# Performance work log

Hardware: AMD Instinct MI355X
Metric: run time of the kernel (lower is better)

## Reference

```python
import jax, jax.numpy as jnp
import numpy as np

B, T, F, U = 256, 512, 128, 1024  # batch, seq_len, feature dim, lstm units


def setup_inputs() -> dict:
    key = jax.random.key(0)
    ks = jax.random.split(key, 11)
    s = jnp.float32(0.05)  # small init so tanh/sigmoid stay in useful range
    f32 = jnp.float32
    return {
        "input_tensor": jax.random.normal(ks[0], (B, T, F), f32),
        # encoder LSTM weights (keras gate order i,f,c,o packed along last axis)
        "enc_Wx": jax.random.normal(ks[1], (F, 4 * U), f32) * s,
        "enc_Wh": jax.random.normal(ks[2], (U, 4 * U), f32) * s,
        "enc_b": jax.random.normal(ks[3], (4 * U,), f32) * s,
        # decoder LSTMCell weights (input dim = U, since it is fed its own output)
        "dec_Wx": jax.random.normal(ks[4], (U, 4 * U), f32) * s,
        "dec_Wh": jax.random.normal(ks[5], (U, 4 * U), f32) * s,
        "dec_b": jax.random.normal(ks[6], (4 * U,), f32) * s,
        # dense1: U -> U with relu; dense2: U -> F linear
        "d1_W": jax.random.normal(ks[7], (U, U), f32) * s,
        "d1_b": jax.random.normal(ks[8], (U,), f32) * s,
        "d2_W": jax.random.normal(ks[9], (U, F), f32) * s,
        "d2_b": jax.random.normal(ks[10], (F,), f32) * s,
    }


def _lstm_step(Wx, Wh, b):
    """Standard keras LSTM cell step. Gate packing order: i, f, g(cand), o."""
    def step(carry, x_t):
        h, c = carry
        z = x_t @ Wx + h @ Wh + b  # [B, 4U]
        i, f, g, o = jnp.split(z, 4, axis=-1)
        c = jax.nn.sigmoid(f) * c + jax.nn.sigmoid(i) * jnp.tanh(g)
        h = jax.nn.sigmoid(o) * jnp.tanh(c)
        return (h, c), h
    return step


def reference(input_tensor, enc_Wx, enc_Wh, enc_b, dec_Wx, dec_Wh, dec_b,
              d1_W, d1_b, d2_W, d2_b):
    x = input_tensor
    b_sz, t_len = x.shape[0], x.shape[1]
    u = enc_Wh.shape[0]
    h0 = jnp.zeros((b_sz, u), x.dtype)

    # Encoder: run LSTM over time, keep only final (h, c) (return_state=True).
    (h, c), _ = jax.lax.scan(_lstm_step(enc_Wx, enc_Wh, enc_b), (h0, h0),
                             jnp.swapaxes(x, 0, 1))  # xs: [T, B, F]

    # Decoder: feed previous output back as input, T steps.
    dec_step = _lstm_step(dec_Wx, dec_Wh, dec_b)
    def dec(carry, _):
        x_in, hh, cc = carry
        (hh, cc), _ = dec_step((hh, cc), x_in)
        return (hh, hh, cc), hh  # next input is the new hidden output

    _, hs = jax.lax.scan(dec, (h, h, c), None, length=t_len)  # hs: [T, B, U]

    # Per-step projections, fused over all timesteps (same math as in-loop dense).
    y = jnp.maximum(hs @ d1_W + d1_b, 0.0) @ d2_W + d2_b  # [T, B, F]
    return jnp.swapaxes(y, 0, 1)  # [B, T, F]
```

## Files before the change

### kernel.cpp

```cpp
#include <hip/hip_runtime.h>
#include <hip/hip_bf16.h>
#include <math.h>
#include <stdio.h>


typedef __attribute__((ext_vector_type(8))) short short8;
typedef __attribute__((ext_vector_type(4))) float f32x4;

#define MFMA(a, b, c) __builtin_amdgcn_mfma_f32_16x16x32_bf16(a, b, c, 0, 0, 0)

__device__ __forceinline__ short f2bf(float f) {
  union { __hip_bfloat16 h; short s; } u;
  u.h = __float2bfloat16(f);
  return u.s;
}
__device__ __forceinline__ void split3(float x, short& a, short& b, short& c) {
  union { __hip_bfloat16 h; short s; } u;
  u.h = __float2bfloat16(x); a = u.s;
  float r1 = x - __bfloat162float(u.h);
  u.h = __float2bfloat16(r1); b = u.s;
  float r2 = r1 - __bfloat162float(u.h);
  u.h = __float2bfloat16(r2); c = u.s;
}
__device__ __forceinline__ float sigm(float x) { return 1.0f / (1.0f + expf(-x)); }

__global__ void pack_w(const float* __restrict__ a, const float* __restrict__ b,
                       short8* __restrict__ dst, int KC, int mode, int ncols,
                       int limbs) {
  int gid = blockIdx.x * 256 + threadIdx.x;
  int lane = gid & 63;
  int kc = (gid >> 6) % KC;
  int nt = gid / (KC * 64);
  int u16 = lane & 15, kq = lane >> 4;
  int kbase = kc * 32 + kq * 8;
  int col;
  if (mode <= 1) { int g = nt & 3, ub = nt >> 2; col = g * 1024 + ub * 16 + u16; }
  else col = nt * 16 + u16;
  short8 v0, v1, v2;
#pragma unroll
  for (int j = 0; j < 8; ++j) {
    int k = kbase + j;
    float x;
    if (mode == 0)      x = a[(size_t)k * 4096 + col] + b[(size_t)k * 4096 + col];
    else if (mode == 1) x = (k < 1024) ? a[(size_t)k * 4096 + col]
                                       : b[(size_t)(k - 1024) * 4096 + col];
    else                x = a[(size_t)k * ncols + col];
    short sa, sb, sc; split3(x, sa, sb, sc);
    v0[j] = sa; v1[j] = sb; v2[j] = sc;
  }
  if (limbs == 3) {
    size_t base = (size_t)(nt * KC + kc) * 3 * 64 + lane;
    dst[base] = v0; dst[base + 64] = v1; dst[base + 128] = v2;
  } else {
    dst[(size_t)(nt * KC + kc) * 64 + lane] = v0;
  }
}

__global__ void pack_x32(const float* __restrict__ src, short8* __restrict__ dst,
                         int t0) {
  int gid = blockIdx.x * 256 + threadIdx.x;
  int lane = gid & 63;
  int kx = (gid >> 6) & 3;
  int mt = (gid >> 8) & 15;
  int tloc = gid >> 12;
  int bb = mt * 16 + (lane & 15);
  int fb = kx * 32 + (lane >> 4) * 8;
  const float* s = src + ((size_t)bb * 512 + (t0 + tloc)) * 128 + fb;
  short8 v0, v1, v2;
#pragma unroll
  for (int j = 0; j < 8; ++j) {
    short sa, sb, sc; split3(s[j], sa, sb, sc);
    v0[j] = sa; v1[j] = sb; v2[j] = sc;
  }
  size_t base = (size_t)((tloc * 16 + mt) * 4 + kx) * 3 * 64 + lane;
  dst[base] = v0; dst[base + 64] = v1; dst[base + 128] = v2;
}

__global__ void zero_f(float* p, int n) {
  int i = blockIdx.x * 256 + threadIdx.x;
  if (i < n) p[i] = 0.f;
}

__global__ __launch_bounds__(512) void lstm_step(
    const short8* __restrict__ Ah, const short8* __restrict__ Ax,
    const short8* __restrict__ W, const float* __restrict__ bias,
    float* __restrict__ cst, short8* __restrict__ Hnext,
    short8* __restrict__ Hring, int KC) {
  int tid = threadIdx.x;
  int lane = tid & 63, wv = tid >> 6;
  int wr = wv & 3, wc = wv >> 2;
  int xcd = blockIdx.x & 7, idx = blockIdx.x >> 3;
  int mb = idx & 3, ub = xcd * 8 + (idx >> 2);
  int mt = mb * 4 + wr;
  int nt0 = ub * 4 + wc * 2, nt1 = nt0 + 1;
  const f32x4 z4 = {0.f, 0.f, 0.f, 0.f};
  f32x4 acc0 = z4, acc1 = z4;
  for (int kc = 0; kc < KC; ++kc) {
    const short8* Ap = (kc < 32)
        ? (Ah + ((size_t)(mt * 32 + kc) * 3) * 64 + lane)
        : (Ax + ((size_t)(mt * 4 + (kc - 32)) * 3) * 64 + lane);
    short8 a0 = Ap[0], a1 = Ap[64], a2 = Ap[128];
    const short8* Bp = W + ((size_t)(nt0 * KC + kc) * 3) * 64 + lane;
    const short8* Bq = W + ((size_t)(nt1 * KC + kc) * 3) * 64 + lane;
    short8 b00 = Bp[0], b01 = Bp[64], b02 = Bp[128];
    short8 b10 = Bq[0], b11 = Bq[64], b12 = Bq[128];
    acc0 = MFMA(a0, b00, acc0);  acc1 = MFMA(a0, b10, acc1);
    acc0 = MFMA(a0, b01, acc0);  acc1 = MFMA(a0, b11, acc1);
    acc0 = MFMA(a1, b00, acc0);  acc1 = MFMA(a1, b10, acc1);
    acc0 = MFMA(a1, b01, acc0);  acc1 = MFMA(a1, b11, acc1);
    acc0 = MFMA(a0, b02, acc0);  acc1 = MFMA(a0, b12, acc1);
    acc0 = MFMA(a2, b00, acc0);  acc1 = MFMA(a2, b10, acc1);
  }

  __shared__ float zt[64][68];
  int u16 = lane & 15, quad = lane >> 4;
  float bv0 = bias[(wc * 2 + 0) * 1024 + ub * 16 + u16];
  float bv1 = bias[(wc * 2 + 1) * 1024 + ub * 16 + u16];
#pragma unroll
  for (int r = 0; r < 4; ++r) {
    zt[wr * 16 + quad * 4 + r][(wc * 2 + 0) * 16 + u16] = acc0[r] + bv0;
    zt[wr * 16 + quad * 4 + r][(wc * 2 + 1) * 16 + u16] = acc1[r] + bv1;
  }
  __syncthreads();

  if (tid < 128) {
    int r = tid >> 1, s = tid & 1;
    int m = mb * 64 + r;
    int ubase = ub * 16 + s * 8;
    float* cp = cst + (size_t)m * 1024 + ubase;
    short8 h0, h1, h2;
#pragma unroll
    for (int j = 0; j < 8; ++j) {
      int uu = s * 8 + j;
      float iv = zt[r][uu];
      float fv = zt[r][16 + uu];
      float gv = zt[r][32 + uu];
      float ov = zt[r][48 + uu];
      float cn = sigm(fv) * cp[j] + sigm(iv) * tanhf(gv);
      cp[j] = cn;
      float hval = sigm(ov) * tanhf(cn);
      short sa, sb, sc; split3(hval, sa, sb, sc);
      h0[j] = sa; h1[j] = sb; h2[j] = sc;
    }
    int mtw = m >> 4, r16 = m & 15;
    int kcw = ubase >> 5, ko = ubase & 31;
    int lane_t = r16 + 16 * (ko >> 3);
    size_t base = ((size_t)(mtw * 32 + kcw) * 3) * 64 + lane_t;
    Hnext[base] = h0; Hnext[base + 64] = h1; Hnext[base + 128] = h2;
    if (Hring)
      Hring[(size_t)(mtw * 32 + kcw) * 64 + lane_t] = h0;
  }
}

__global__ __launch_bounds__(256) void proj(
    const short8* __restrict__ HS, const short8* __restrict__ W1,
    const float* __restrict__ b1, const short8* __restrict__ W2,
    const float* __restrict__ b2, float* __restrict__ out, int t0) {
  int tid = threadIdx.x;
  int lane = tid & 63, wv = tid >> 6;
  int wr = wv & 1, wc = wv >> 1;
  int tloc = blockIdx.x >> 2, mb = blockIdx.x & 3;
  int t = t0 + tloc;
  const short8* A = HS + (size_t)tloc * 16 * 32 * 64;
  int u16 = lane & 15, quad = lane >> 4;
  int mt0 = mb * 4 + wr * 2;
  __shared__ short a1f[4][8][512];
  const f32x4 z4 = {0.f, 0.f, 0.f, 0.f};
  f32x4 acc2[2][4];
#pragma unroll
  for (int i = 0; i < 2; ++i)
#pragma unroll
    for (int jj = 0; jj < 4; ++jj) acc2[i][jj] = z4;

  for (int q = 0; q < 4; ++q) {
    f32x4 acc1[2][8];
#pragma unroll
    for (int i = 0; i < 2; ++i)
#pragma unroll
      for (int n = 0; n < 8; ++n) acc1[i][n] = z4;
    for (int kc = 0; kc < 32; ++kc) {
      short8 av0 = A[(size_t)(mt0 * 32 + kc) * 64 + lane];
      short8 av1 = A[(size_t)((mt0 + 1) * 32 + kc) * 64 + lane];
#pragma unroll
      for (int n = 0; n < 8; ++n) {
        int nt = q * 16 + wc * 8 + n;
        short8 bv = W1[(size_t)(nt * 32 + kc) * 64 + lane];
        acc1[0][n] = MFMA(av0, bv, acc1[0][n]);
        acc1[1][n] = MFMA(av1, bv, acc1[1][n]);
      }
    }
    __syncthreads();
#pragma unroll
    for (int i = 0; i < 2; ++i)
#pragma unroll
      for (int n = 0; n < 8; ++n)
#pragma unroll
        for (int r = 0; r < 4; ++r) {
          int rl = wr * 32 + i * 16 + quad * 4 + r;
          int nloc = wc * 128 + n * 16 + u16;
          float v = fmaxf(acc1[i][n][r] + b1[q * 256 + nloc], 0.f);
          int mtl = rl >> 4, r16 = rl & 15;
          int kcl = nloc >> 5, ko = nloc & 31;
          a1f[mtl][kcl][(r16 + 16 * (ko >> 3)) * 8 + (ko & 7)] = f2bf(v);
        }
    __syncthreads();
    for (int kcl = 0; kcl < 8; ++kcl) {
      short8 av0 = *(const short8*)&a1f[wr * 2 + 0][kcl][lane * 8];
      short8 av1 = *(const short8*)&a1f[wr * 2 + 1][kcl][lane * 8];
#pragma unroll
      for (int jj = 0; jj < 4; ++jj) {
        int nt2 = wc * 4 + jj;
        short8 bv = W2[(size_t)(nt2 * 32 + q * 8 + kcl) * 64 + lane];
        acc2[0][jj] = MFMA(av0, bv, acc2[0][jj]);
        acc2[1][jj] = MFMA(av1, bv, acc2[1][jj]);
      }
    }
  }
#pragma unroll
  for (int i = 0; i < 2; ++i)
#pragma unroll
    for (int jj = 0; jj < 4; ++jj)
#pragma unroll
      for (int r = 0; r < 4; ++r) {
        int rl = wr * 32 + i * 16 + quad * 4 + r;
        int f = wc * 64 + jj * 16 + u16;
        int bb = mb * 64 + rl;
        out[((size_t)bb * 512 + t) * 128 + f] = acc2[i][jj][r] + b2[f];
      }
}

extern "C" void kernel_launch(void* const* d_in, const int* in_sizes, int n_in,
                              void* d_out, int out_size, void* d_ws, size_t ws_size,
                              hipStream_t stream) {
  const float* x     = (const float*)d_in[0];
  const float* encWx = (const float*)d_in[1];
  const float* encWh = (const float*)d_in[2];
  const float* encb  = (const float*)d_in[3];
  const float* decWx = (const float*)d_in[4];
  const float* decWh = (const float*)d_in[5];
  const float* decb  = (const float*)d_in[6];
  const float* d1W   = (const float*)d_in[7];
  const float* d1b   = (const float*)d_in[8];
  const float* d2W   = (const float*)d_in[9];
  const float* d2b   = (const float*)d_in[10];

  char* ws = (char*)d_ws;
  size_t off = 0;
  short8* Wenc = (short8*)(ws + off); off += (size_t)256 * 36 * 3 * 64 * 16;
  short8* Wdec = (short8*)(ws + off); off += (size_t)256 * 32 * 3 * 64 * 16;
  short8* W1   = (short8*)(ws + off); off += (size_t)64 * 32 * 64 * 16;
  short8* W2   = (short8*)(ws + off); off += (size_t)8 * 32 * 64 * 16;
  short8* Xr   = (short8*)(ws + off); off += (size_t)32 * 16 * 4 * 3 * 64 * 16;
  short8* Hb   = (short8*)(ws + off); off += (size_t)2 * 16 * 32 * 3 * 64 * 16;
  short8* Hring= (short8*)(ws + off); off += (size_t)32 * 16 * 32 * 64 * 16;
  float*  cst  = (float*)(ws + off);  off += (size_t)256 * 1024 * 4;
  (void)in_sizes; (void)n_in; (void)out_size;
  if (ws_size < off) {
    fprintf(stderr, "kernel_launch: ws_size=%zu < needed=%zu -- aborting launch\n",
            ws_size, off);
    return;
  }

  pack_w<<<2304, 256, 0, stream>>>(encWh, encWx, Wenc, 36, 1, 4096, 3);
  pack_w<<<2048, 256, 0, stream>>>(decWx, decWh, Wdec, 32, 0, 4096, 3);
  pack_w<<<512, 256, 0, stream>>>(d1W, nullptr, W1, 32, 2, 1024, 1);
  pack_w<<<64, 256, 0, stream>>>(d2W, nullptr, W2, 32, 3, 128, 1);
  zero_f<<<1536, 256, 0, stream>>>((float*)Hb, 16 * 32 * 3 * 64 * 8);
  zero_f<<<1024, 256, 0, stream>>>(cst, 256 * 1024);

  const size_t H3 = (size_t)16 * 32 * 3 * 64;
  const size_t XT = (size_t)16 * 4 * 3 * 64;
  const size_t HR = (size_t)16 * 32 * 64;

  for (int c = 0; c < 16; ++c) {
    pack_x32<<<512, 256, 0, stream>>>(x, Xr, c * 32);
    for (int i = 0; i < 32; ++i) {
      int t = c * 32 + i;
      lstm_step<<<256, 512, 0, stream>>>(Hb + (size_t)(t & 1) * H3, Xr + (size_t)i * XT,
                                         Wenc, encb, cst,
                                         Hb + (size_t)((t + 1) & 1) * H3, nullptr, 36);
    }
  }
  for (int c = 0; c < 16; ++c) {
    for (int i = 0; i < 32; ++i) {
      int d = c * 32 + i;
      lstm_step<<<256, 512, 0, stream>>>(Hb + (size_t)(d & 1) * H3, nullptr,
                                         Wdec, decb, cst,
                                         Hb + (size_t)((d + 1) & 1) * H3,
                                         Hring + (size_t)i * HR, 32);
    }
    proj<<<128, 256, 0, stream>>>(Hring, W1, d1b, W2, d2b, (float*)d_out, c * 32);
  }
}
```

Measured before the change: 38.12 ms.

## Fuse all LSTM steps and projections into one persistent kernel with grid barriers

Replaces about 1040 per-timestep kernel launches with a single persistent kernel of 256 blocks that loops over all encoder and decoder steps and synchronises through a flag-based global barrier. Cell state is kept in registers instead of global memory. The input x is split into bf16 limbs inline rather than by a separate pack kernel, and the dense projections run inside the same kernel every 32 decoder steps. Each block now covers a 64-row by 64-column gate tile with 256 threads rather than 512. This removes launch overhead and global c-state traffic. The cost is spin-wait barrier latency, and the design depends on all 256 blocks being resident at the same time.

```diff
diff --git a/kernel.cpp b/kernel.cpp
--- a/kernel.cpp
+++ b/kernel.cpp
@@ -8,6 +8,11 @@
 typedef __attribute__((ext_vector_type(4))) float f32x4;
 
 #define MFMA(a, b, c) __builtin_amdgcn_mfma_f32_16x16x32_bf16(a, b, c, 0, 0, 0)
+
+#define LIMB6(acc, A0, A1, A2, B0, B1, B2) \
+  acc = MFMA(A0, B0, acc); acc = MFMA(A0, B1, acc); \
+  acc = MFMA(A1, B0, acc); acc = MFMA(A1, B1, acc); \
+  acc = MFMA(A0, B2, acc); acc = MFMA(A2, B0, acc);
 
 __device__ __forceinline__ short f2bf(float f) {
   union { __hip_bfloat16 h; short s; } u;
@@ -56,177 +61,221 @@
   }
 }
 
-__global__ void pack_x32(const float* __restrict__ src, short8* __restrict__ dst,
-                         int t0) {
-  int gid = blockIdx.x * 256 + threadIdx.x;
-  int lane = gid & 63;
-  int kx = (gid >> 6) & 3;
-  int mt = (gid >> 8) & 15;
-  int tloc = gid >> 12;
-  int bb = mt * 16 + (lane & 15);
-  int fb = kx * 32 + (lane >> 4) * 8;
-  const float* s = src + ((size_t)bb * 512 + (t0 + tloc)) * 128 + fb;
-  short8 v0, v1, v2;
-#pragma unroll
-  for (int j = 0; j < 8; ++j) {
-    short sa, sb, sc; split3(s[j], sa, sb, sc);
-    v0[j] = sa; v1[j] = sb; v2[j] = sc;
-  }
-  size_t base = (size_t)((tloc * 16 + mt) * 4 + kx) * 3 * 64 + lane;
-  dst[base] = v0; dst[base + 64] = v1; dst[base + 128] = v2;
-}
-
 __global__ void zero_f(float* p, int n) {
   int i = blockIdx.x * 256 + threadIdx.x;
   if (i < n) p[i] = 0.f;
 }
 
-__global__ __launch_bounds__(512) void lstm_step(
-    const short8* __restrict__ Ah, const short8* __restrict__ Ax,
-    const short8* __restrict__ W, const float* __restrict__ bias,
-    float* __restrict__ cst, short8* __restrict__ Hnext,
-    short8* __restrict__ Hring, int KC) {
-  int tid = threadIdx.x;
-  int lane = tid & 63, wv = tid >> 6;
-  int wr = wv & 3, wc = wv >> 2;
-  int xcd = blockIdx.x & 7, idx = blockIdx.x >> 3;
-  int mb = idx & 3, ub = xcd * 8 + (idx >> 2);
-  int mt = mb * 4 + wr;
-  int nt0 = ub * 4 + wc * 2, nt1 = nt0 + 1;
-  const f32x4 z4 = {0.f, 0.f, 0.f, 0.f};
-  f32x4 acc0 = z4, acc1 = z4;
-  for (int kc = 0; kc < KC; ++kc) {
-    const short8* Ap = (kc < 32)
-        ? (Ah + ((size_t)(mt * 32 + kc) * 3) * 64 + lane)
-        : (Ax + ((size_t)(mt * 4 + (kc - 32)) * 3) * 64 + lane);
-    short8 a0 = Ap[0], a1 = Ap[64], a2 = Ap[128];
-    const short8* Bp = W + ((size_t)(nt0 * KC + kc) * 3) * 64 + lane;
-    const short8* Bq = W + ((size_t)(nt1 * KC + kc) * 3) * 64 + lane;
-    short8 b00 = Bp[0], b01 = Bp[64], b02 = Bp[128];
-    short8 b10 = Bq[0], b11 = Bq[64], b12 = Bq[128];
-    acc0 = MFMA(a0, b00, acc0);  acc1 = MFMA(a0, b10, acc1);
-    acc0 = MFMA(a0, b01, acc0);  acc1 = MFMA(a0, b11, acc1);
-    acc0 = MFMA(a1, b00, acc0);  acc1 = MFMA(a1, b10, acc1);
-    acc0 = MFMA(a1, b01, acc0);  acc1 = MFMA(a1, b11, acc1);
-    acc0 = MFMA(a0, b02, acc0);  acc1 = MFMA(a0, b12, acc1);
-    acc0 = MFMA(a2, b00, acc0);  acc1 = MFMA(a2, b10, acc1);
-  }
-
-  __shared__ float zt[64][68];
-  int u16 = lane & 15, quad = lane >> 4;
-  float bv0 = bias[(wc * 2 + 0) * 1024 + ub * 16 + u16];
-  float bv1 = bias[(wc * 2 + 1) * 1024 + ub * 16 + u16];
-#pragma unroll
-  for (int r = 0; r < 4; ++r) {
-    zt[wr * 16 + quad * 4 + r][(wc * 2 + 0) * 16 + u16] = acc0[r] + bv0;
-    zt[wr * 16 + quad * 4 + r][(wc * 2 + 1) * 16 + u16] = acc1[r] + bv1;
-  }
+__device__ __forceinline__ void gbar(int* flags, int bid, int gen) {
   __syncthreads();
-
-  if (tid < 128) {
-    int r = tid >> 1, s = tid & 1;
-    int m = mb * 64 + r;
-    int ubase = ub * 16 + s * 8;
-    float* cp = cst + (size_t)m * 1024 + ubase;
-    short8 h0, h1, h2;
-#pragma unroll
-    for (int j = 0; j < 8; ++j) {
-      int uu = s * 8 + j;
-      float iv = zt[r][uu];
-      float fv = zt[r][16 + uu];
-      float gv = zt[r][32 + uu];
-      float ov = zt[r][48 + uu];
-      float cn = sigm(fv) * cp[j] + sigm(iv) * tanhf(gv);
-      cp[j] = cn;
-      float hval = sigm(ov) * tanhf(cn);
-      short sa, sb, sc; split3(hval, sa, sb, sc);
-      h0[j] = sa; h1[j] = sb; h2[j] = sc;
-    }
-    int mtw = m >> 4, r16 = m & 15;
-    int kcw = ubase >> 5, ko = ubase & 31;
-    int lane_t = r16 + 16 * (ko >> 3);
-    size_t base = ((size_t)(mtw * 32 + kcw) * 3) * 64 + lane_t;
-    Hnext[base] = h0; Hnext[base + 64] = h1; Hnext[base + 128] = h2;
-    if (Hring)
-      Hring[(size_t)(mtw * 32 + kcw) * 64 + lane_t] = h0;
-  }
-}
-
-__global__ __launch_bounds__(256) void proj(
-    const short8* __restrict__ HS, const short8* __restrict__ W1,
-    const float* __restrict__ b1, const short8* __restrict__ W2,
-    const float* __restrict__ b2, float* __restrict__ out, int t0) {
-  int tid = threadIdx.x;
+  if (threadIdx.x == 0) {
+    __builtin_amdgcn_fence(__ATOMIC_RELEASE, "agent");
+    __hip_atomic_store(&flags[bid], gen, __ATOMIC_RELAXED, __HIP_MEMORY_SCOPE_AGENT);
+  }
+  int v;
+  do {
+    v = __hip_atomic_load(&flags[threadIdx.x], __ATOMIC_RELAXED,
+                          __HIP_MEMORY_SCOPE_AGENT);
+    if (v < gen) __builtin_amdgcn_s_sleep(2);
+  } while (v < gen);
+  __builtin_amdgcn_fence(__ATOMIC_ACQUIRE, "agent");
+  __syncthreads();
+}
+
+__global__ __launch_bounds__(256) void lstm_all(
+    const float* __restrict__ x,
+    const short8* __restrict__ Wenc, const float* __restrict__ encb,
+    const short8* __restrict__ Wdec, const float* __restrict__ decb,
+    const short8* __restrict__ W1, const float* __restrict__ b1,
+    const short8* __restrict__ W2, const float* __restrict__ b2,
+    short8* __restrict__ Hb, short8* __restrict__ Hring,
+    int* __restrict__ flags, float* __restrict__ out) {
+
+  __shared__ union {
+    float zt[64][68];
+    short a1f[4][8][512];
+  } sh;
+
+  int tid = threadIdx.x, bid = blockIdx.x;
   int lane = tid & 63, wv = tid >> 6;
   int wr = wv & 1, wc = wv >> 1;
-  int tloc = blockIdx.x >> 2, mb = blockIdx.x & 3;
-  int t = t0 + tloc;
-  const short8* A = HS + (size_t)tloc * 16 * 32 * 64;
+  int xcd = bid & 7, idx = bid >> 3;
+  int rb = idx >> 3;
+  int ub = xcd * 8 + (idx & 7);
   int u16 = lane & 15, quad = lane >> 4;
-  int mt0 = mb * 4 + wr * 2;
-  __shared__ short a1f[4][8][512];
-  const f32x4 z4 = {0.f, 0.f, 0.f, 0.f};
-  f32x4 acc2[2][4];
-#pragma unroll
-  for (int i = 0; i < 2; ++i)
-#pragma unroll
-    for (int jj = 0; jj < 4; ++jj) acc2[i][jj] = z4;
-
-  for (int q = 0; q < 4; ++q) {
-    f32x4 acc1[2][8];
-#pragma unroll
-    for (int i = 0; i < 2; ++i)
-#pragma unroll
-      for (int n = 0; n < 8; ++n) acc1[i][n] = z4;
+  int gen = 0;
+
+  float c8[8];
+#pragma unroll
+  for (int j = 0; j < 8; ++j) c8[j] = 0.f;
+
+  const size_t H3 = (size_t)16 * 32 * 3 * 64;
+  const size_t HR = (size_t)16 * 32 * 64;
+  const int mt0 = rb * 4 + wr * 2;
+  const int nt0 = ub * 4 + wc * 2;
+
+  for (int step = 0; step < 1024; ++step) {
+    const bool enc = step < 512;
+    const int t = enc ? step : step - 512;
+    const short8* A = Hb + (size_t)(step & 1) * H3;
+    short8* Ho = Hb + (size_t)((step + 1) & 1) * H3;
+    const short8* W = enc ? Wenc : Wdec;
+    const float* bias = enc ? encb : decb;
+    const int KC = enc ? 36 : 32;
+
+    const f32x4 z4 = {0.f, 0.f, 0.f, 0.f};
+    f32x4 acc00 = z4, acc01 = z4, acc10 = z4, acc11 = z4;
+    const short8* Ap0 = A + (size_t)mt0 * 32 * 3 * 64 + lane;
+    const short8* Ap1 = A + (size_t)(mt0 + 1) * 32 * 3 * 64 + lane;
+    const short8* Bp0 = W + (size_t)nt0 * KC * 3 * 64 + lane;
+    const short8* Bp1 = W + (size_t)(nt0 + 1) * KC * 3 * 64 + lane;
+
     for (int kc = 0; kc < 32; ++kc) {
-      short8 av0 = A[(size_t)(mt0 * 32 + kc) * 64 + lane];
-      short8 av1 = A[(size_t)((mt0 + 1) * 32 + kc) * 64 + lane];
-#pragma unroll
-      for (int n = 0; n < 8; ++n) {
-        int nt = q * 16 + wc * 8 + n;
-        short8 bv = W1[(size_t)(nt * 32 + kc) * 64 + lane];
-        acc1[0][n] = MFMA(av0, bv, acc1[0][n]);
-        acc1[1][n] = MFMA(av1, bv, acc1[1][n]);
+      short8 a00 = Ap0[kc * 192], a01 = Ap0[kc * 192 + 64], a02 = Ap0[kc * 192 + 128];
+      short8 a10 = Ap1[kc * 192], a11 = Ap1[kc * 192 + 64], a12 = Ap1[kc * 192 + 128];
+      short8 b00 = Bp0[kc * 192], b01 = Bp0[kc * 192 + 64], b02 = Bp0[kc * 192 + 128];
+      short8 b10 = Bp1[kc * 192], b11 = Bp1[kc * 192 + 64], b12 = Bp1[kc * 192 + 128];
+      LIMB6(acc00, a00, a01, a02, b00, b01, b02);
+      LIMB6(acc01, a00, a01, a02, b10, b11, b12);
+      LIMB6(acc10, a10, a11, a12, b00, b01, b02);
+      LIMB6(acc11, a10, a11, a12, b10, b11, b12);
+    }
+    if (enc) {
+#pragma unroll
+      for (int kx = 0; kx < 4; ++kx) {
+        int kc = 32 + kx;
+        short8 xa0[2], xa1[2], xa2[2];
+#pragma unroll
+        for (int i = 0; i < 2; ++i) {
+          const float* xp = x + ((size_t)((mt0 + i) * 16 + u16) * 512 + t) * 128
+                              + kx * 32 + quad * 8;
+#pragma unroll
+          for (int j = 0; j < 8; ++j) {
+            short sa, sb, sc; split3(xp[j], sa, sb, sc);
+            xa0[i][j] = sa; xa1[i][j] = sb; xa2[i][j] = sc;
+          }
+        }
+        short8 b00 = Bp0[kc * 192], b01 = Bp0[kc * 192 + 64], b02 = Bp0[kc * 192 + 128];
+        short8 b10 = Bp1[kc * 192], b11 = Bp1[kc * 192 + 64], b12 = Bp1[kc * 192 + 128];
+        LIMB6(acc00, xa0[0], xa1[0], xa2[0], b00, b01, b02);
+        LIMB6(acc01, xa0[0], xa1[0], xa2[0], b10, b11, b12);
+        LIMB6(acc10, xa0[1], xa1[1], xa2[1], b00, b01, b02);
+        LIMB6(acc11, xa0[1], xa1[1], xa2[1], b10, b11, b12);
       }
     }
+
+    float bv0 = bias[(wc * 2 + 0) * 1024 + ub * 16 + u16];
+    float bv1 = bias[(wc * 2 + 1) * 1024 + ub * 16 + u16];
+#pragma unroll
+    for (int r = 0; r < 4; ++r) {
+      sh.zt[wr * 32 + 0 * 16 + quad * 4 + r][(wc * 2 + 0) * 16 + u16] = acc00[r] + bv0;
+      sh.zt[wr * 32 + 0 * 16 + quad * 4 + r][(wc * 2 + 1) * 16 + u16] = acc01[r] + bv1;
+      sh.zt[wr * 32 + 1 * 16 + quad * 4 + r][(wc * 2 + 0) * 16 + u16] = acc10[r] + bv0;
+      sh.zt[wr * 32 + 1 * 16 + quad * 4 + r][(wc * 2 + 1) * 16 + u16] = acc11[r] + bv1;
+    }
     __syncthreads();
-#pragma unroll
-    for (int i = 0; i < 2; ++i)
-#pragma unroll
-      for (int n = 0; n < 8; ++n)
-#pragma unroll
-        for (int r = 0; r < 4; ++r) {
-          int rl = wr * 32 + i * 16 + quad * 4 + r;
-          int nloc = wc * 128 + n * 16 + u16;
-          float v = fmaxf(acc1[i][n][r] + b1[q * 256 + nloc], 0.f);
-          int mtl = rl >> 4, r16 = rl & 15;
-          int kcl = nloc >> 5, ko = nloc & 31;
-          a1f[mtl][kcl][(r16 + 16 * (ko >> 3)) * 8 + (ko & 7)] = f2bf(v);
+
+    if (tid < 128) {
+      int r = tid >> 1, s = tid & 1;
+      int m = rb * 64 + r;
+      int ubase = ub * 16 + s * 8;
+      short8 h0, h1, h2;
+#pragma unroll
+      for (int j = 0; j < 8; ++j) {
+        int uu = s * 8 + j;
+        float iv = sh.zt[r][uu];
+        float fv = sh.zt[r][16 + uu];
+        float gv = sh.zt[r][32 + uu];
+        float ov = sh.zt[r][48 + uu];
+        float cn = sigm(fv) * c8[j] + sigm(iv) * tanhf(gv);
+        c8[j] = cn;
+        float hval = sigm(ov) * tanhf(cn);
+        short sa, sb, sc; split3(hval, sa, sb, sc);
+        h0[j] = sa; h1[j] = sb; h2[j] = sc;
+      }
+      int mtw = m >> 4, r16 = m & 15;
+      int kcw = ubase >> 5, ko = ubase & 31;
+      int lane_t = r16 + 16 * (ko >> 3);
+      size_t base = ((size_t)(mtw * 32 + kcw) * 3) * 64 + lane_t;
+      Ho[base] = h0; Ho[base + 64] = h1; Ho[base + 128] = h2;
+      if (!enc)
+        Hring[(size_t)(t & 31) * HR + (size_t)(mtw * 32 + kcw) * 64 + lane_t] = h0;
+    }
+
+    gbar(flags, bid, ++gen);
+
+    if (!enc && (t & 31) == 31) {
+      if (bid < 128) {
+        int tloc = bid >> 2, mb = bid & 3;
+        int tt = (t - 31) + tloc;
+        const short8* Ah = Hring + (size_t)tloc * HR;
+        int pmt0 = mb * 4 + wr * 2;
+        const f32x4 pz = {0.f, 0.f, 0.f, 0.f};
+        f32x4 acc2[2][4];
+#pragma unroll
+        for (int i = 0; i < 2; ++i)
+#pragma unroll
+          for (int jj = 0; jj < 4; ++jj) acc2[i][jj] = pz;
+
+        for (int q = 0; q < 4; ++q) {
+          f32x4 acc1[2][8];
+#pragma unroll
+          for (int i = 0; i < 2; ++i)
+#pragma unroll
+            for (int n = 0; n < 8; ++n) acc1[i][n] = pz;
+          for (int kc = 0; kc < 32; ++kc) {
+            short8 av0 = Ah[(size_t)(pmt0 * 32 + kc) * 64 + lane];
+            short8 av1 = Ah[(size_t)((pmt0 + 1) * 32 + kc) * 64 + lane];
+#pragma unroll
+            for (int n = 0; n < 8; ++n) {
+              int nt = q * 16 + wc * 8 + n;
+              short8 bv = W1[(size_t)(nt * 32 + kc) * 64 + lane];
+              acc1[0][n] = MFMA(av0, bv, acc1[0][n]);
+              acc1[1][n] = MFMA(av1, bv, acc1[1][n]);
+            }
+          }
+          __syncthreads();
+#pragma unroll
+          for (int i = 0; i < 2; ++i)
+#pragma unroll
+            for (int n = 0; n < 8; ++n)
+#pragma unroll
+              for (int r = 0; r < 4; ++r) {
+                int rl = wr * 32 + i * 16 + quad * 4 + r;
+                int nloc = wc * 128 + n * 16 + u16;
+                float v = fmaxf(acc1[i][n][r] + b1[q * 256 + nloc], 0.f);
+                int mtl = rl >> 4, r16 = rl & 15;
+                int kcl = nloc >> 5, ko = nloc & 31;
+                sh.a1f[mtl][kcl][(r16 + 16 * (ko >> 3)) * 8 + (ko & 7)] = f2bf(v);
+              }
+          __syncthreads();
+          for (int kcl = 0; kcl < 8; ++kcl) {
+            short8 av0 = *(const short8*)&sh.a1f[wr * 2 + 0][kcl][lane * 8];
+            short8 av1 = *(const short8*)&sh.a1f[wr * 2 + 1][kcl][lane * 8];
+#pragma unroll
+            for (int jj = 0; jj < 4; ++jj) {
+              int nt2 = wc * 4 + jj;
+              short8 bv = W2[(size_t)(nt2 * 32 + q * 8 + kcl) * 64 + lane];
+              acc2[0][jj] = MFMA(av0, bv, acc2[0][jj]);
+              acc2[1][jj] = MFMA(av1, bv, acc2[1][jj]);
+            }
+          }
         }
-    __syncthreads();
-    for (int kcl = 0; kcl < 8; ++kcl) {
-      short8 av0 = *(const short8*)&a1f[wr * 2 + 0][kcl][lane * 8];
-      short8 av1 = *(const short8*)&a1f[wr * 2 + 1][kcl][lane * 8];
-#pragma unroll
-      for (int jj = 0; jj < 4; ++jj) {
-        int nt2 = wc * 4 + jj;
-        short8 bv = W2[(size_t)(nt2 * 32 + q * 8 + kcl) * 64 + lane];
-        acc2[0][jj] = MFMA(av0, bv, acc2[0][jj]);
-        acc2[1][jj] = MFMA(av1, bv, acc2[1][jj]);
+#pragma unroll
+        for (int i = 0; i < 2; ++i)
+#pragma unroll
+          for (int jj = 0; jj < 4; ++jj)
+#pragma unroll
+            for (int r = 0; r < 4; ++r) {
+              int rl = wr * 32 + i * 16 + quad * 4 + r;
+              int f = wc * 64 + jj * 16 + u16;
+              int bb = mb * 64 + rl;
+              out[((size_t)bb * 512 + tt) * 128 + f] = acc2[i][jj][r] + b2[f];
+            }
       }
-    }
-  }
-#pragma unroll
-  for (int i = 0; i < 2; ++i)
-#pragma unroll
-    for (int jj = 0; jj < 4; ++jj)
-#pragma unroll
-      for (int r = 0; r < 4; ++r) {
-        int rl = wr * 32 + i * 16 + quad * 4 + r;
-        int f = wc * 64 + jj * 16 + u16;
-        int bb = mb * 64 + rl;
-        out[((size_t)bb * 512 + t) * 128 + f] = acc2[i][jj][r] + b2[f];
-      }
+      gbar(flags, bid, ++gen);
+    }
+  }
 }
 
 extern "C" void kernel_launch(void* const* d_in, const int* in_sizes, int n_in,
@@ -250,10 +299,9 @@
   short8* Wdec = (short8*)(ws + off); off += (size_t)256 * 32 * 3 * 64 * 16;
   short8* W1   = (short8*)(ws + off); off += (size_t)64 * 32 * 64 * 16;
   short8* W2   = (short8*)(ws + off); off += (size_t)8 * 32 * 64 * 16;
-  short8* Xr   = (short8*)(ws + off); off += (size_t)32 * 16 * 4 * 3 * 64 * 16;
   short8* Hb   = (short8*)(ws + off); off += (size_t)2 * 16 * 32 * 3 * 64 * 16;
   short8* Hring= (short8*)(ws + off); off += (size_t)32 * 16 * 32 * 64 * 16;
-  float*  cst  = (float*)(ws + off);  off += (size_t)256 * 1024 * 4;
+  int*   flags = (int*)(ws + off);    off += 1024;
   (void)in_sizes; (void)n_in; (void)out_size;
   if (ws_size < off) {
     fprintf(stderr, "kernel_launch: ws_size=%zu < needed=%zu -- aborting launch\n",
@@ -265,30 +313,9 @@
   pack_w<<<2048, 256, 0, stream>>>(decWx, decWh, Wdec, 32, 0, 4096, 3);
   pack_w<<<512, 256, 0, stream>>>(d1W, nullptr, W1, 32, 2, 1024, 1);
   pack_w<<<64, 256, 0, stream>>>(d2W, nullptr, W2, 32, 3, 128, 1);
-  zero_f<<<1536, 256, 0, stream>>>((float*)Hb, 16 * 32 * 3 * 64 * 8);
-  zero_f<<<1024, 256, 0, stream>>>(cst, 256 * 1024);
-
-  const size_t H3 = (size_t)16 * 32 * 3 * 64;
-  const size_t XT = (size_t)16 * 4 * 3 * 64;
-  const size_t HR = (size_t)16 * 32 * 64;
-
-  for (int c = 0; c < 16; ++c) {
-    pack_x32<<<512, 256, 0, stream>>>(x, Xr, c * 32);
-    for (int i = 0; i < 32; ++i) {
-      int t = c * 32 + i;
-      lstm_step<<<256, 512, 0, stream>>>(Hb + (size_t)(t & 1) * H3, Xr + (size_t)i * XT,
-                                         Wenc, encb, cst,
-                                         Hb + (size_t)((t + 1) & 1) * H3, nullptr, 36);
-    }
-  }
-  for (int c = 0; c < 16; ++c) {
-    for (int i = 0; i < 32; ++i) {
-      int d = c * 32 + i;
-      lstm_step<<<256, 512, 0, stream>>>(Hb + (size_t)(d & 1) * H3, nullptr,
-                                         Wdec, decb, cst,
-                                         Hb + (size_t)((d + 1) & 1) * H3,
-                                         Hring + (size_t)i * HR, 32);
-    }
-    proj<<<128, 256, 0, stream>>>(Hring, W1, d1b, W2, d2b, (float*)d_out, c * 32);
-  }
-}
+  zero_f<<<3072, 256, 0, stream>>>((float*)Hb, 786432);
+  zero_f<<<1, 256, 0, stream>>>((float*)flags, 256);
+
+  lstm_all<<<256, 256, 0, stream>>>(x, Wenc, encb, Wdec, decb, W1, d1b, W2, d2b,
+                                    Hb, Hring, flags, (float*)d_out);
+}
```

Result: slower. 49.96 ms (+31.1%).
